# Kernel tuning notes

Measured on AMD Instinct MI355X. Metric: run time of the kernel, lower is better.

## Reference

```python
import jax, jax.numpy as jnp
import numpy as np

P, K, H, D = 64, 8, 32, 2048   # ids_per_batch, imgs_per_id, local stripes, feature dim
MARGIN = 10.0


def _euclid(x, y):
    # x: [m, d], y: [n, d] -> [m, n]
    xx = jnp.sum(x * x, axis=1, keepdims=True)          # [m, 1]
    yy = jnp.sum(y * y, axis=1)[None, :]                # [1, n]
    d2 = xx + yy - 2.0 * (x @ y.T)
    return jnp.sqrt(jnp.clip(d2, 1e-12, None))


def _shortest_dist(dmat):
    # dmat: [m, n, *rest]; DP: dist[i,j] = dmat[i,j] + min(dist[i-1,j], dist[i,j-1])
    m, n = dmat.shape[0], dmat.shape[1]
    rest = dmat.shape[2:]
    d = dmat.reshape(m, n, -1)                          # [m, n, B]
    B = d.shape[2]
    # virtual row above: +inf everywhere except col 0 (so dist[0,0] = dmat[0,0])
    prev0 = jnp.full((n, B), jnp.inf, d.dtype).at[0].set(0.0)

    def row_step(prev_row, drow):
        def col_step(left, ud):
            up, dd = ud
            cur = jnp.minimum(up, left) + dd
            return cur, cur
        _, row = jax.lax.scan(col_step, jnp.full((B,), jnp.inf, d.dtype), (prev_row, drow))
        return row, None

    last_row, _ = jax.lax.scan(row_step, prev0, d)
    return last_row[-1].reshape(rest)                   # dist at (m-1, n-1)


def _local_dist(x, y):
    # x: [M, m, d], y: [N, n, d] -> [M, N]
    M, m, d = x.shape
    N, n, _ = y.shape
    dm = _euclid(x.reshape(M * m, d), y.reshape(N * n, d))
    dm = jnp.tanh(dm * 0.5)                             # (e^d - 1) / (e^d + 1)
    dm = dm.reshape(M, m, N, n).transpose(1, 3, 0, 2)   # [m, n, M, N]
    return _shortest_dist(dm)                           # [M, N]


def setup_inputs() -> dict:
    key = jax.random.key(0)
    features = jax.random.normal(key, (P * K, H, D), dtype=jnp.float32)
    targets = jnp.arange(P * K, dtype=jnp.int32) // K   # ordered p*k labels
    return {"features": features, "targets": targets}


def reference(features, targets):
    # ordered p*k batch: classes are contiguous blocks of K
    feats = features.reshape(P, K, H, D)
    centers = feats.mean(axis=1)                        # [P, H, D]

    # intra: center vs its K members -> max over members, per class
    intra_max = jax.vmap(lambda c, f: _local_dist(c[None], f).max())(centers, feats)  # [P]

    # inter: center vs all other centers -> min over others, per class
    inter_full = _local_dist(centers, centers)          # [P, P]
    eye = jnp.eye(P, dtype=bool)
    inter_min = jnp.where(eye, jnp.inf, inter_full).min(axis=1)  # [P]

    loss = jnp.mean(jax.nn.relu(intra_max - inter_min + MARGIN))
    return loss, intra_max, inter_min
```

## Files before the change

### kernel.cpp

```cpp
#include <hip/hip_runtime.h>
#include <hip/hip_fp8.h>
#include <cstdint>
#include <cstddef>

#define PP 64
#define KK 8
#define HH 32
#define DD 2048
#define RR (PP*HH)

typedef __attribute__((ext_vector_type(4))) float  f32x4;
typedef __attribute__((ext_vector_type(4))) float  float4v;

__device__ __forceinline__ unsigned int f2fp8(float f) {
  return (unsigned int)__hip_fp8_e4m3(f).__x;
}

__device__ __forceinline__ void gload_lds16(const void* g, void* l) {
  __builtin_amdgcn_global_load_lds(
      (const __attribute__((address_space(1))) void*)g,
      (__attribute__((address_space(3))) void*)l, 16, 0, 0);
}

__device__ __forceinline__ float dp_wave(const float* tile, int j32, int stride) {
  const float INF = __builtin_inff();
  float A = INF;
  for (int d = 0; d < 63; ++d) {
    float left = __shfl_up(A, 1, 32);
    if (j32 == 0) left = INF;
    int i = d - j32;
    int ii = i < 0 ? 0 : (i > 31 ? 31 : i);
    float dv = tile[ii*stride + j32];
    float up = (i == 0) ? (j32 == 0 ? 0.f : INF) : A;
    A = (i >= 0 && i < 32) ? (fminf(up, left) + dv) : INF;
  }
  return A;
}

__global__ __launch_bounds__(256) void k_centers(const float* __restrict__ feat,
    unsigned char* __restrict__ cbf, unsigned char* __restrict__ fbf,
    float* __restrict__ cnorm, float* __restrict__ fnorm) {
  int row = blockIdx.x;
  int p = row >> 5, h = row & 31;
  int tid = threadIdx.x;
  int d0 = tid * 8;
  float c[8];
  float red[9];
  #pragma unroll
  for (int e = 0; e < 8; ++e) c[e] = 0.f;
  #pragma unroll
  for (int k = 0; k < KK; ++k) {
    size_t frow = (size_t)((p*KK + k)*HH + h);
    const float* src = feat + frow*DD + d0;
    float4v f0 = *(const float4v*)src;
    float4v f1 = *(const float4v*)(src + 4);
    float s = 0.f;
    #pragma unroll
    for (int e = 0; e < 4; ++e) {
      c[e]   += f0[e];
      c[4+e] += f1[e];
      s += f0[e]*f0[e] + f1[e]*f1[e];
    }
    red[k] = s;
    unsigned int lo = f2fp8(f0[0]) | (f2fp8(f0[1])<<8) | (f2fp8(f0[2])<<16) | (f2fp8(f0[3])<<24);
    unsigned int hi = f2fp8(f1[0]) | (f2fp8(f1[1])<<8) | (f2fp8(f1[2])<<16) | (f2fp8(f1[3])<<24);
    *(uint2*)(fbf + frow*DD + d0) = make_uint2(lo, hi);
  }
  float csq = 0.f;
  #pragma unroll
  for (int e = 0; e < 8; ++e) { c[e] *= 0.125f; csq += c[e]*c[e]; }
  {
    unsigned int lo = f2fp8(c[0]) | (f2fp8(c[1])<<8) | (f2fp8(c[2])<<16) | (f2fp8(c[3])<<24);
    unsigned int hi = f2fp8(c[4]) | (f2fp8(c[5])<<8) | (f2fp8(c[6])<<16) | (f2fp8(c[7])<<24);
    *(uint2*)(cbf + (size_t)row*DD + d0) = make_uint2(lo, hi);
  }
  red[8] = csq;

  __shared__ float lred[4][9];
  int lane = tid & 63, wv = tid >> 6;
  #pragma unroll
  for (int r = 0; r < 9; ++r) {
    float v = red[r];
    #pragma unroll
    for (int off = 32; off > 0; off >>= 1) v += __shfl_down(v, off, 64);
    if (lane == 0) lred[wv][r] = v;
  }
  __syncthreads();
  if (tid < 9) {
    float s = lred[0][tid] + lred[1][tid] + lred[2][tid] + lred[3][tid];
    if (tid < 8) fnorm[((size_t)(p*KK + tid))*HH + h] = s;
    else         cnorm[row] = s;
  }
}

__global__ __launch_bounds__(256) void k_gram(const unsigned char* __restrict__ cbf,
    const unsigned char* __restrict__ fbf, const float* __restrict__ cnorm,
    const float* __restrict__ fnorm, float* __restrict__ inter_full,
    float* __restrict__ intra_pk) {
  __shared__ char smem[24576];
  int tid = threadIdx.x, lane = tid & 63, w = tid >> 6;
  int ln = lane & 15, kq = lane >> 4;
  int cch = (lane & 3) ^ ((lane >> 3) & 3);

  if (blockIdx.x < 528) {
    int bid = (blockIdx.x & 7)*66 + (blockIdx.x >> 3);
    int tI = 0, rem = bid;
    while (rem >= 32 - tI) { rem -= 32 - tI; ++tI; }
    int tJ = tI + rem;
    int wr = w >> 1, wc = w & 1;
    f32x4 acc[2][2];
    #pragma unroll
    for (int a = 0; a < 2; ++a)
      #pragma unroll
      for (int b = 0; b < 2; ++b)
        #pragma unroll
        for (int e = 0; e < 4; ++e) acc[a][b][e] = 0.f;

    const unsigned char* gA0 = cbf + (size_t)(tI*64 + w*16 + (lane >> 2))*DD + cch*16;
    const unsigned char* gB0 = cbf + (size_t)(tJ*64 + w*16 + (lane >> 2))*DD + cch*16;

    int aofs[2][2], bofs[2][2];
    #pragma unroll
    for (int ks = 0; ks < 2; ++ks) {
      int phys = ((ks*4 + kq) ^ (ln & 6))*8;
      #pragma unroll
      for (int mt = 0; mt < 2; ++mt) {
        aofs[ks][mt] = (wr*32 + mt*16 + ln)*64 + phys;
        bofs[ks][mt] = (wc*32 + mt*16 + ln)*64 + phys;
      }
    }

    auto stage = [&](int tt, int bi) {
      int k0 = tt * 64;
      char* A = smem + bi*8192;
      gload_lds16(gA0 + k0, A + w*1024 + lane*16);
      gload_lds16(gB0 + k0, A + 4096 + w*1024 + lane*16);
    };
    auto do_step = [&](int bi) {
      const char* A = smem + bi*8192;
      const char* B = A + 4096;
      #pragma unroll
      for (int ks = 0; ks < 2; ++ks) {
        long long af[2], bf[2];
        #pragma unroll
        for (int mt = 0; mt < 2; ++mt) {
          af[mt] = *(const long long*)(A + aofs[ks][mt]);
          bf[mt] = *(const long long*)(B + bofs[ks][mt]);
        }
        #pragma unroll
        for (int mt = 0; mt < 2; ++mt)
          #pragma unroll
          for (int nt = 0; nt < 2; ++nt)
            acc[mt][nt] = __builtin_amdgcn_mfma_f32_16x16x32_fp8_fp8(af[mt], bf[nt], acc[mt][nt], 0, 0, 0);
      }
    };

    stage(0, 0);
    stage(1, 1);
    asm volatile("s_waitcnt vmcnt(2)" ::: "memory");
    __builtin_amdgcn_s_barrier();
    for (int t = 0; t < 30; ++t) {
      stage(t + 2, (t + 2) % 3);
      do_step(t % 3);
      asm volatile("s_waitcnt vmcnt(2)" ::: "memory");
      __builtin_amdgcn_s_barrier();
    }
    do_step(0);
    asm volatile("s_waitcnt vmcnt(0)" ::: "memory");
    __builtin_amdgcn_s_barrier();
    do_step(1);
    __syncthreads();

    int a = tI*2 + wr, b = tJ*2 + wc;
    bool own = (a < b);
    float* tile = (float*)(smem + w*4096);
    if (own) {
      #pragma unroll
      for (int mt = 0; mt < 2; ++mt) {
        #pragma unroll
        for (int nt = 0; nt < 2; ++nt) {
          int j  = nt*16 + ln;
          int cc = tJ*64 + wc*32 + j;
          float nc = cnorm[cc];
          #pragma unroll
          for (int v = 0; v < 4; ++v) {
            int i  = mt*16 + kq*4 + v;
            int rr = tI*64 + wr*32 + i;
            float d2 = cnorm[rr] + nc - 2.f*acc[mt][nt][v];
            tile[(i << 5) + j] = tanhf(0.5f*sqrtf(fmaxf(d2, 1e-12f)));
          }
        }
      }
    }
    __syncthreads();
    if (own) {
      float A = dp_wave(tile, lane & 31, 32);
      if (lane == 31) {
        inter_full[a*64 + b] = A;
        inter_full[b*64 + a] = A;
      }
    }
  } else {
    int bid = (int)blockIdx.x - 528;
    int p = bid >> 3, jb = bid & 7;
    int ks = w >> 1, nt = w & 1;
    f32x4 acc[2];
    #pragma unroll
    for (int mi = 0; mi < 2; ++mi)
      #pragma unroll
      for (int e = 0; e < 4; ++e) acc[mi][e] = 0.f;

    int hw = w & 1;
    const unsigned char* g0 = (w < 2)
        ? cbf + (size_t)(p*32 + hw*16 + (lane >> 2))*DD + cch*16
        : fbf + (size_t)(p*256 + jb*32 + hw*16 + (lane >> 2))*DD + cch*16;
    int isB = (w >= 2);

    int phys = ((ks*4 + kq) ^ (ln & 6))*8;
    int aofs[2];
    #pragma unroll
    for (int mi = 0; mi < 2; ++mi) aofs[mi] = (mi*16 + ln)*64 + phys;
    int bofs = (nt*16 + ln)*64 + phys;

    auto stage = [&](int tt, int bi) {
      int k0 = tt * 64;
      char* S = smem + bi*4096 + isB*2048;
      gload_lds16(g0 + k0, S + hw*1024 + lane*16);
    };
    auto do_step = [&](int bi) {
      const char* A = smem + bi*4096;
      const char* B = A + 2048;
      long long bfr = *(const long long*)(B + bofs);
      #pragma unroll
      for (int mi = 0; mi < 2; ++mi) {
        long long af = *(const long long*)(A + aofs[mi]);
        acc[mi] = __builtin_amdgcn_mfma_f32_16x16x32_fp8_fp8(af, bfr, acc[mi], 0, 0, 0);
      }
    };

    stage(0, 0);
    stage(1, 1);
    asm volatile("s_waitcnt vmcnt(1)" ::: "memory");
    __builtin_amdgcn_s_barrier();
    for (int t = 0; t < 30; ++t) {
      stage(t + 2, (t + 2) % 3);
      do_step(t % 3);
      asm volatile("s_waitcnt vmcnt(1)" ::: "memory");
      __builtin_amdgcn_s_barrier();
    }
    do_step(0);
    asm volatile("s_waitcnt vmcnt(0)" ::: "memory");
    __builtin_amdgcn_s_barrier();
    do_step(1);

    float* fb = (float*)smem;
    float* tile = (float*)(smem + 16384);
    __syncthreads();
    if (w >= 2) {
      #pragma unroll
      for (int mi = 0; mi < 2; ++mi)
        *(f32x4*)(fb + ((w - 2)*2 + mi)*256 + lane*4) = acc[mi];
    }
    __syncthreads();
    if (w < 2) {
      #pragma unroll
      for (int mi = 0; mi < 2; ++mi)
        acc[mi] += *(const f32x4*)(fb + (w*2 + mi)*256 + lane*4);
      int cl = jb*32 + nt*16 + ln;
      float nf = fnorm[(size_t)p*256 + cl];
      #pragma unroll
      for (int mi = 0; mi < 2; ++mi) {
        #pragma unroll
        for (int v = 0; v < 4; ++v) {
          int i = mi*16 + kq*4 + v;
          float d2 = cnorm[p*32 + i] + nf - 2.f*acc[mi][v];
          tile[(i << 5) + (nt*16 + ln)] = tanhf(0.5f*sqrtf(fmaxf(d2, 1e-12f)));
        }
      }
    }
    __syncthreads();
    if (w == 0) {
      float A = dp_wave(tile, lane & 31, 32);
      if (lane == 31) intra_pk[p*8 + jb] = A;
    }
  }
}

__global__ __launch_bounds__(64) void k_final(const float* __restrict__ inter_full,
    const float* __restrict__ intra_pk, float* __restrict__ out) {
  int p = threadIdx.x;
  const float INF = __builtin_inff();
  float mn = INF;
  #pragma unroll 8
  for (int b = 0; b < 64; ++b)
    if (b != p) mn = fminf(mn, inter_full[p*64 + b]);
  float mx = -INF;
  #pragma unroll
  for (int k = 0; k < 8; ++k) mx = fmaxf(mx, intra_pk[p*8 + k]);
  out[1 + p]  = mx;
  out[65 + p] = mn;
  float v = fmaxf(mx - mn + 10.0f, 0.0f);
  #pragma unroll
  for (int off = 32; off > 0; off >>= 1) v += __shfl_down(v, off, 64);
  if (p == 0) out[0] = v * (1.0f/64.0f);
}

extern "C" void kernel_launch(void* const* d_in, const int* in_sizes, int n_in,
                              void* d_out, int out_size, void* d_ws, size_t ws_size,
                              hipStream_t stream) {
  const float* feat = (const float*)d_in[0];
  float* out = (float*)d_out;
  char* w = (char*)d_ws;
  unsigned char* cbf  = (unsigned char*)w;
  unsigned char* fbf  = (unsigned char*)(w + 4194304);
  float* cnorm        = (float*)(w + 37748736);
  float* fnorm        = (float*)(w + 37756928);
  float* inter_full   = (float*)(w + 37822464);
  float* intra_pk     = (float*)(w + 37838848);

  k_centers<<<RR, 256, 0, stream>>>(feat, cbf, fbf, cnorm, fnorm);
  k_gram<<<1040, 256, 0, stream>>>(cbf, fbf, cnorm, fnorm, inter_full, intra_pk);
  k_final<<<1, 64, 0, stream>>>(inter_full, intra_pk, out);
}
```

Before: 67.24 us.

## Double-buffer 128-wide K stages in gram kernel and fuse final reduction via ticket

The gram kernel's K loop changes from a triple-buffered 64-byte step with a partial wait to a double-buffered 128-byte step: each stage issues twice as many loads and each barrier now covers two MFMA halves, halving the barrier count. The separate final-reduction kernel is removed. Instead, the last gram block to finish, detected with an atomic ticket that k_centers resets, computes the loss, intra max and inter min. This saves a kernel launch but adds an atomic and a fence per block and a full vmcnt(0) wait each iteration.

```diff
diff --git a/kernel.cpp b/kernel.cpp
--- a/kernel.cpp
+++ b/kernel.cpp
@@ -8,6 +8,7 @@
 #define HH 32
 #define DD 2048
 #define RR (PP*HH)
+#define NBLK 1040
 
 typedef __attribute__((ext_vector_type(4))) float  f32x4;
 typedef __attribute__((ext_vector_type(4))) float  float4v;
@@ -22,7 +23,7 @@
       (__attribute__((address_space(3))) void*)l, 16, 0, 0);
 }
 
-__device__ __forceinline__ float dp_wave(const float* tile, int j32, int stride) {
+__device__ __forceinline__ float dp_wave(const float* tile, int j32) {
   const float INF = __builtin_inff();
   float A = INF;
   for (int d = 0; d < 63; ++d) {
@@ -30,7 +31,7 @@
     if (j32 == 0) left = INF;
     int i = d - j32;
     int ii = i < 0 ? 0 : (i > 31 ? 31 : i);
-    float dv = tile[ii*stride + j32];
+    float dv = tile[(ii << 5) + j32];
     float up = (i == 0) ? (j32 == 0 ? 0.f : INF) : A;
     A = (i >= 0 && i < 32) ? (fminf(up, left) + dv) : INF;
   }
@@ -39,10 +40,12 @@
 
 __global__ __launch_bounds__(256) void k_centers(const float* __restrict__ feat,
     unsigned char* __restrict__ cbf, unsigned char* __restrict__ fbf,
-    float* __restrict__ cnorm, float* __restrict__ fnorm) {
+    float* __restrict__ cnorm, float* __restrict__ fnorm,
+    unsigned int* __restrict__ ticket) {
   int row = blockIdx.x;
   int p = row >> 5, h = row & 31;
   int tid = threadIdx.x;
+  if (row == 0 && tid == 0) atomicExch(ticket, 0u);
   int d0 = tid * 8;
   float c[8];
   float red[9];
@@ -96,8 +99,9 @@
 __global__ __launch_bounds__(256) void k_gram(const unsigned char* __restrict__ cbf,
     const unsigned char* __restrict__ fbf, const float* __restrict__ cnorm,
     const float* __restrict__ fnorm, float* __restrict__ inter_full,
-    float* __restrict__ intra_pk) {
-  __shared__ char smem[24576];
+    float* __restrict__ intra_pk, unsigned int* __restrict__ ticket,
+    float* __restrict__ out) {
+  __shared__ char smem[32768];
   int tid = threadIdx.x, lane = tid & 63, w = tid >> 6;
   int ln = lane & 15, kq = lane >> 4;
   int cch = (lane & 3) ^ ((lane >> 3) & 3);
@@ -130,14 +134,16 @@
       }
     }
 
-    auto stage = [&](int tt, int bi) {
-      int k0 = tt * 64;
-      char* A = smem + bi*8192;
-      gload_lds16(gA0 + k0, A + w*1024 + lane*16);
-      gload_lds16(gB0 + k0, A + 4096 + w*1024 + lane*16);
+    auto stage = [&](int e, int bi) {
+      int k0 = e * 128;
+      char* buf = smem + bi*16384;
+      gload_lds16(gA0 + k0,      buf +         w*1024 + lane*16);
+      gload_lds16(gB0 + k0,      buf +  4096 + w*1024 + lane*16);
+      gload_lds16(gA0 + k0 + 64, buf +  8192 + w*1024 + lane*16);
+      gload_lds16(gB0 + k0 + 64, buf + 12288 + w*1024 + lane*16);
     };
-    auto do_step = [&](int bi) {
-      const char* A = smem + bi*8192;
+    auto do_half = [&](int bi, int half) {
+      const char* A = smem + bi*16384 + half*8192;
       const char* B = A + 4096;
       #pragma unroll
       for (int ks = 0; ks < 2; ++ks) {
@@ -156,19 +162,19 @@
     };
 
     stage(0, 0);
-    stage(1, 1);
-    asm volatile("s_waitcnt vmcnt(2)" ::: "memory");
-    __builtin_amdgcn_s_barrier();
-    for (int t = 0; t < 30; ++t) {
-      stage(t + 2, (t + 2) % 3);
-      do_step(t % 3);
-      asm volatile("s_waitcnt vmcnt(2)" ::: "memory");
-      __builtin_amdgcn_s_barrier();
-    }
-    do_step(0);
     asm volatile("s_waitcnt vmcnt(0)" ::: "memory");
     __builtin_amdgcn_s_barrier();
-    do_step(1);
+    int cur = 0;
+    for (int e = 0; e < 15; ++e) {
+      stage(e + 1, cur ^ 1);
+      do_half(cur, 0);
+      do_half(cur, 1);
+      asm volatile("s_waitcnt vmcnt(0)" ::: "memory");
+      __builtin_amdgcn_s_barrier();
+      cur ^= 1;
+    }
+    do_half(cur, 0);
+    do_half(cur, 1);
     __syncthreads();
 
     int a = tI*2 + wr, b = tJ*2 + wc;
@@ -194,7 +200,7 @@
     }
     __syncthreads();
     if (own) {
-      float A = dp_wave(tile, lane & 31, 32);
+      float A = dp_wave(tile, lane & 31);
       if (lane == 31) {
         inter_full[a*64 + b] = A;
         inter_full[b*64 + a] = A;
@@ -222,13 +228,14 @@
     for (int mi = 0; mi < 2; ++mi) aofs[mi] = (mi*16 + ln)*64 + phys;
     int bofs = (nt*16 + ln)*64 + phys;
 
-    auto stage = [&](int tt, int bi) {
-      int k0 = tt * 64;
-      char* S = smem + bi*4096 + isB*2048;
-      gload_lds16(g0 + k0, S + hw*1024 + lane*16);
+    auto stage = [&](int e, int bi) {
+      int k0 = e * 128;
+      char* buf = smem + bi*8192;
+      gload_lds16(g0 + k0,      buf +        isB*2048 + hw*1024 + lane*16);
+      gload_lds16(g0 + k0 + 64, buf + 4096 + isB*2048 + hw*1024 + lane*16);
     };
-    auto do_step = [&](int bi) {
-      const char* A = smem + bi*4096;
+    auto do_half = [&](int bi, int half) {
+      const char* A = smem + bi*8192 + half*4096;
       const char* B = A + 2048;
       long long bfr = *(const long long*)(B + bofs);
       #pragma unroll
@@ -239,19 +246,19 @@
     };
 
     stage(0, 0);
-    stage(1, 1);
-    asm volatile("s_waitcnt vmcnt(1)" ::: "memory");
-    __builtin_amdgcn_s_barrier();
-    for (int t = 0; t < 30; ++t) {
-      stage(t + 2, (t + 2) % 3);
-      do_step(t % 3);
-      asm volatile("s_waitcnt vmcnt(1)" ::: "memory");
-      __builtin_amdgcn_s_barrier();
-    }
-    do_step(0);
     asm volatile("s_waitcnt vmcnt(0)" ::: "memory");
     __builtin_amdgcn_s_barrier();
-    do_step(1);
+    int cur = 0;
+    for (int e = 0; e < 15; ++e) {
+      stage(e + 1, cur ^ 1);
+      do_half(cur, 0);
+      do_half(cur, 1);
+      asm volatile("s_waitcnt vmcnt(0)" ::: "memory");
+      __builtin_amdgcn_s_barrier();
+      cur ^= 1;
+    }
+    do_half(cur, 0);
+    do_half(cur, 1);
 
     float* fb = (float*)smem;
     float* tile = (float*)(smem + 16384);
@@ -280,29 +287,41 @@
     }
     __syncthreads();
     if (w == 0) {
-      float A = dp_wave(tile, lane & 31, 32);
+      float A = dp_wave(tile, lane & 31);
       if (lane == 31) intra_pk[p*8 + jb] = A;
     }
   }
-}
-
-__global__ __launch_bounds__(64) void k_final(const float* __restrict__ inter_full,
-    const float* __restrict__ intra_pk, float* __restrict__ out) {
-  int p = threadIdx.x;
-  const float INF = __builtin_inff();
-  float mn = INF;
-  #pragma unroll 8
-  for (int b = 0; b < 64; ++b)
-    if (b != p) mn = fminf(mn, inter_full[p*64 + b]);
-  float mx = -INF;
-  #pragma unroll
-  for (int k = 0; k < 8; ++k) mx = fmaxf(mx, intra_pk[p*8 + k]);
-  out[1 + p]  = mx;
-  out[65 + p] = mn;
-  float v = fmaxf(mx - mn + 10.0f, 0.0f);
-  #pragma unroll
-  for (int off = 32; off > 0; off >>= 1) v += __shfl_down(v, off, 64);
-  if (p == 0) out[0] = v * (1.0f/64.0f);
+
+  __threadfence();
+  __syncthreads();
+  volatile int* flag = (int*)(smem + 28672);
+  if (tid == 0) {
+    unsigned int old = atomicAdd(ticket, 1u);
+    if (old == NBLK - 1) {
+      __threadfence();
+      *flag = 1;
+    } else {
+      *flag = 0;
+    }
+  }
+  __syncthreads();
+  if (*flag && tid < 64) {
+    int p = tid;
+    const float INF = __builtin_inff();
+    float mn = INF;
+    #pragma unroll 8
+    for (int b = 0; b < 64; ++b)
+      if (b != p) mn = fminf(mn, inter_full[p*64 + b]);
+    float mx = -INF;
+    #pragma unroll
+    for (int k = 0; k < 8; ++k) mx = fmaxf(mx, intra_pk[p*8 + k]);
+    out[1 + p]  = mx;
+    out[65 + p] = mn;
+    float v = fmaxf(mx - mn + 10.0f, 0.0f);
+    #pragma unroll
+    for (int off = 32; off > 0; off >>= 1) v += __shfl_down(v, off, 64);
+    if (p == 0) out[0] = v * (1.0f/64.0f);
+  }
 }
 
 extern "C" void kernel_launch(void* const* d_in, const int* in_sizes, int n_in,
@@ -317,8 +336,8 @@
   float* fnorm        = (float*)(w + 37756928);
   float* inter_full   = (float*)(w + 37822464);
   float* intra_pk     = (float*)(w + 37838848);
-
-  k_centers<<<RR, 256, 0, stream>>>(feat, cbf, fbf, cnorm, fnorm);
-  k_gram<<<1040, 256, 0, stream>>>(cbf, fbf, cnorm, fnorm, inter_full, intra_pk);
-  k_final<<<1, 64, 0, stream>>>(inter_full, intra_pk, out);
-}
+  unsigned int* ticket= (unsigned int*)(w + 37840896);
+
+  k_centers<<<RR, 256, 0, stream>>>(feat, cbf, fbf, cnorm, fnorm, ticket);
+  k_gram<<<NBLK, 256, 0, stream>>>(cbf, fbf, cnorm, fnorm, inter_full, intra_pk, ticket, out);
+}
```

New measurement: 133.9 us. +99.2%, slower.

## Enlarge inter-center gram tiles to 128x128 and pre-swizzle fp8 layout in producer

Applied to the files above, without the earlier changes.

The center-center gram blocks grow from 64x64 to 128x128 tiles with 4x4 MFMA accumulators per wave, cutting the inter grid from 528 to 136 blocks and raising operand reuse per LDS load. The fp8 XOR swizzle moves from the gram loader into the k_centers store, so gram loads become plain contiguous 16-byte chunks. Each wave now runs its four 32x32 DP sub-tiles serially without block barriers, using a padded stride of 33. The cost is more registers, doubled LDS, and fewer blocks, which may hurt occupancy and leave the inter portion with less parallelism.

```diff
diff --git a/kernel.cpp b/kernel.cpp
--- a/kernel.cpp
+++ b/kernel.cpp
@@ -44,6 +44,8 @@
   int p = row >> 5, h = row & 31;
   int tid = threadIdx.x;
   int d0 = tid * 8;
+  int s = (row >> 1) & 7;
+  int wofs = (tid >> 3)*64 + ((tid & 7) ^ s)*8;
   float c[8];
   float red[9];
   #pragma unroll
@@ -54,17 +56,17 @@
     const float* src = feat + frow*DD + d0;
     float4v f0 = *(const float4v*)src;
     float4v f1 = *(const float4v*)(src + 4);
-    float s = 0.f;
+    float sacc = 0.f;
     #pragma unroll
     for (int e = 0; e < 4; ++e) {
       c[e]   += f0[e];
       c[4+e] += f1[e];
-      s += f0[e]*f0[e] + f1[e]*f1[e];
-    }
-    red[k] = s;
+      sacc += f0[e]*f0[e] + f1[e]*f1[e];
+    }
+    red[k] = sacc;
     unsigned int lo = f2fp8(f0[0]) | (f2fp8(f0[1])<<8) | (f2fp8(f0[2])<<16) | (f2fp8(f0[3])<<24);
     unsigned int hi = f2fp8(f1[0]) | (f2fp8(f1[1])<<8) | (f2fp8(f1[2])<<16) | (f2fp8(f1[3])<<24);
-    *(uint2*)(fbf + frow*DD + d0) = make_uint2(lo, hi);
+    *(uint2*)(fbf + frow*DD + wofs) = make_uint2(lo, hi);
   }
   float csq = 0.f;
   #pragma unroll
@@ -72,7 +74,7 @@
   {
     unsigned int lo = f2fp8(c[0]) | (f2fp8(c[1])<<8) | (f2fp8(c[2])<<16) | (f2fp8(c[3])<<24);
     unsigned int hi = f2fp8(c[4]) | (f2fp8(c[5])<<8) | (f2fp8(c[6])<<16) | (f2fp8(c[7])<<24);
-    *(uint2*)(cbf + (size_t)row*DD + d0) = make_uint2(lo, hi);
+    *(uint2*)(cbf + (size_t)row*DD + wofs) = make_uint2(lo, hi);
   }
   red[8] = csq;
 
@@ -87,9 +89,9 @@
   }
   __syncthreads();
   if (tid < 9) {
-    float s = lred[0][tid] + lred[1][tid] + lred[2][tid] + lred[3][tid];
-    if (tid < 8) fnorm[((size_t)(p*KK + tid))*HH + h] = s;
-    else         cnorm[row] = s;
+    float sum = lred[0][tid] + lred[1][tid] + lred[2][tid] + lred[3][tid];
+    if (tid < 8) fnorm[((size_t)(p*KK + tid))*HH + h] = sum;
+    else         cnorm[row] = sum;
   }
 }
 
@@ -97,72 +99,73 @@
     const unsigned char* __restrict__ fbf, const float* __restrict__ cnorm,
     const float* __restrict__ fnorm, float* __restrict__ inter_full,
     float* __restrict__ intra_pk) {
-  __shared__ char smem[24576];
+  __shared__ char smem[49152];
   int tid = threadIdx.x, lane = tid & 63, w = tid >> 6;
   int ln = lane & 15, kq = lane >> 4;
-  int cch = (lane & 3) ^ ((lane >> 3) & 3);
-
-  if (blockIdx.x < 528) {
-    int bid = (blockIdx.x & 7)*66 + (blockIdx.x >> 3);
+
+  if (blockIdx.x < 136) {
+    int bid = (blockIdx.x & 7)*17 + (blockIdx.x >> 3);
     int tI = 0, rem = bid;
-    while (rem >= 32 - tI) { rem -= 32 - tI; ++tI; }
+    while (rem >= 16 - tI) { rem -= 16 - tI; ++tI; }
     int tJ = tI + rem;
     int wr = w >> 1, wc = w & 1;
-    f32x4 acc[2][2];
-    #pragma unroll
-    for (int a = 0; a < 2; ++a)
-      #pragma unroll
-      for (int b = 0; b < 2; ++b)
+    f32x4 acc[4][4];
+    #pragma unroll
+    for (int a = 0; a < 4; ++a)
+      #pragma unroll
+      for (int b = 0; b < 4; ++b)
         #pragma unroll
         for (int e = 0; e < 4; ++e) acc[a][b][e] = 0.f;
 
-    const unsigned char* gA0 = cbf + (size_t)(tI*64 + w*16 + (lane >> 2))*DD + cch*16;
-    const unsigned char* gB0 = cbf + (size_t)(tJ*64 + w*16 + (lane >> 2))*DD + cch*16;
-
-    int aofs[2][2], bofs[2][2];
+    const unsigned char* gA0 = cbf + (size_t)(tI*128 + w*32 + (lane >> 2))*DD + (lane & 3)*16;
+    const unsigned char* gB0 = cbf + (size_t)(tJ*128 + w*32 + (lane >> 2))*DD + (lane & 3)*16;
+
+    int aofs[2][4], bofs[2][4];
     #pragma unroll
     for (int ks = 0; ks < 2; ++ks) {
-      int phys = ((ks*4 + kq) ^ (ln & 6))*8;
-      #pragma unroll
-      for (int mt = 0; mt < 2; ++mt) {
-        aofs[ks][mt] = (wr*32 + mt*16 + ln)*64 + phys;
-        bofs[ks][mt] = (wc*32 + mt*16 + ln)*64 + phys;
+      int phys = ((ks*4 + kq) ^ (ln >> 1))*8;
+      #pragma unroll
+      for (int mt = 0; mt < 4; ++mt) {
+        aofs[ks][mt] = (wr*64 + mt*16 + ln)*64 + phys;
+        bofs[ks][mt] = (wc*64 + mt*16 + ln)*64 + phys;
       }
     }
 
     auto stage = [&](int tt, int bi) {
       int k0 = tt * 64;
-      char* A = smem + bi*8192;
-      gload_lds16(gA0 + k0, A + w*1024 + lane*16);
-      gload_lds16(gB0 + k0, A + 4096 + w*1024 + lane*16);
+      char* A = smem + bi*16384;
+      gload_lds16(gA0 + k0,         A + w*2048 + lane*16);
+      gload_lds16(gA0 + 16*DD + k0, A + w*2048 + 1024 + lane*16);
+      gload_lds16(gB0 + k0,         A + 8192 + w*2048 + lane*16);
+      gload_lds16(gB0 + 16*DD + k0, A + 8192 + w*2048 + 1024 + lane*16);
     };
     auto do_step = [&](int bi) {
-      const char* A = smem + bi*8192;
-      const char* B = A + 4096;
+      const char* A = smem + bi*16384;
+      const char* B = A + 8192;
       #pragma unroll
       for (int ks = 0; ks < 2; ++ks) {
-        long long af[2], bf[2];
-        #pragma unroll
-        for (int mt = 0; mt < 2; ++mt) {
+        long long af[4], bf[4];
+        #pragma unroll
+        for (int mt = 0; mt < 4; ++mt) {
           af[mt] = *(const long long*)(A + aofs[ks][mt]);
           bf[mt] = *(const long long*)(B + bofs[ks][mt]);
         }
         #pragma unroll
-        for (int mt = 0; mt < 2; ++mt)
+        for (int mt = 0; mt < 4; ++mt)
           #pragma unroll
-          for (int nt = 0; nt < 2; ++nt)
+          for (int nt = 0; nt < 4; ++nt)
             acc[mt][nt] = __builtin_amdgcn_mfma_f32_16x16x32_fp8_fp8(af[mt], bf[nt], acc[mt][nt], 0, 0, 0);
       }
     };
 
     stage(0, 0);
     stage(1, 1);
-    asm volatile("s_waitcnt vmcnt(2)" ::: "memory");
+    asm volatile("s_waitcnt vmcnt(4)" ::: "memory");
     __builtin_amdgcn_s_barrier();
     for (int t = 0; t < 30; ++t) {
       stage(t + 2, (t + 2) % 3);
       do_step(t % 3);
-      asm volatile("s_waitcnt vmcnt(2)" ::: "memory");
+      asm volatile("s_waitcnt vmcnt(4)" ::: "memory");
       __builtin_amdgcn_s_barrier();
     }
     do_step(0);
@@ -171,37 +174,42 @@
     do_step(1);
     __syncthreads();
 
-    int a = tI*2 + wr, b = tJ*2 + wc;
-    bool own = (a < b);
-    float* tile = (float*)(smem + w*4096);
-    if (own) {
-      #pragma unroll
-      for (int mt = 0; mt < 2; ++mt) {
-        #pragma unroll
-        for (int nt = 0; nt < 2; ++nt) {
-          int j  = nt*16 + ln;
-          int cc = tJ*64 + wc*32 + j;
-          float nc = cnorm[cc];
+    float* tile = (float*)(smem + w*4352);
+    #pragma unroll
+    for (int ia = 0; ia < 2; ++ia) {
+      #pragma unroll
+      for (int ib = 0; ib < 2; ++ib) {
+        int a = tI*4 + wr*2 + ia;
+        int b = tJ*4 + wc*2 + ib;
+        if (a >= b) continue;
+        #pragma unroll
+        for (int m2 = 0; m2 < 2; ++m2) {
           #pragma unroll
-          for (int v = 0; v < 4; ++v) {
-            int i  = mt*16 + kq*4 + v;
-            int rr = tI*64 + wr*32 + i;
-            float d2 = cnorm[rr] + nc - 2.f*acc[mt][nt][v];
-            tile[(i << 5) + j] = tanhf(0.5f*sqrtf(fmaxf(d2, 1e-12f)));
+          for (int n2 = 0; n2 < 2; ++n2) {
+            int mt = ia*2 + m2, nt = ib*2 + n2;
+            int j  = n2*16 + ln;
+            int cc = tJ*128 + wc*64 + nt*16 + ln;
+            float nc = cnorm[cc];
+            #pragma unroll
+            for (int v = 0; v < 4; ++v) {
+              int i  = m2*16 + kq*4 + v;
+              int rr = tI*128 + wr*64 + mt*16 + kq*4 + v;
+              float d2 = cnorm[rr] + nc - 2.f*acc[mt][nt][v];
+              tile[i*33 + j] = tanhf(0.5f*sqrtf(fmaxf(d2, 1e-12f)));
+            }
           }
         }
-      }
-    }
-    __syncthreads();
-    if (own) {
-      float A = dp_wave(tile, lane & 31, 32);
-      if (lane == 31) {
-        inter_full[a*64 + b] = A;
-        inter_full[b*64 + a] = A;
+        asm volatile("s_waitcnt lgkmcnt(0)" ::: "memory");
+        __builtin_amdgcn_sched_barrier(0);
+        float A = dp_wave(tile, lane & 31, 33);
+        if (lane == 31) {
+          inter_full[a*64 + b] = A;
+          inter_full[b*64 + a] = A;
+        }
       }
     }
   } else {
-    int bid = (int)blockIdx.x - 528;
+    int bid = (int)blockIdx.x - 136;
     int p = bid >> 3, jb = bid & 7;
     int ks = w >> 1, nt = w & 1;
     f32x4 acc[2];
@@ -212,11 +220,11 @@
 
     int hw = w & 1;
     const unsigned char* g0 = (w < 2)
-        ? cbf + (size_t)(p*32 + hw*16 + (lane >> 2))*DD + cch*16
-        : fbf + (size_t)(p*256 + jb*32 + hw*16 + (lane >> 2))*DD + cch*16;
+        ? cbf + (size_t)(p*32 + hw*16 + (lane >> 2))*DD + (lane & 3)*16
+        : fbf + (size_t)(p*256 + jb*32 + hw*16 + (lane >> 2))*DD + (lane & 3)*16;
     int isB = (w >= 2);
 
-    int phys = ((ks*4 + kq) ^ (ln & 6))*8;
+    int phys = ((ks*4 + kq) ^ (ln >> 1))*8;
     int aofs[2];
     #pragma unroll
     for (int mi = 0; mi < 2; ++mi) aofs[mi] = (mi*16 + ln)*64 + phys;
@@ -319,6 +327,6 @@
   float* intra_pk     = (float*)(w + 37838848);
 
   k_centers<<<RR, 256, 0, stream>>>(feat, cbf, fbf, cnorm, fnorm);
-  k_gram<<<1040, 256, 0, stream>>>(cbf, fbf, cnorm, fnorm, inter_full, intra_pk);
+  k_gram<<<648, 256, 0, stream>>>(cbf, fbf, cnorm, fnorm, inter_full, intra_pk);
   k_final<<<1, 64, 0, stream>>>(inter_full, intra_pk, out);
 }
```

Result: slower. 99.44 us (+47.9%).
